# Optimization experiments

Hardware: AMD Instinct MI355X
Metric: run time of the kernel (lower is better)

Reference implementation:

```python
import jax, jax.numpy as jnp
import numpy as np

D_MODEL = 1024
N_HEADS = 16
HEAD_DIM = D_MODEL // N_HEADS  # 64
SCALE = HEAD_DIM ** -0.5       # nn.Parameter, frozen since lsa=False


def setup_inputs() -> dict:
    key = jax.random.key(0)
    kq, kk, kv = jax.random.split(key, 3)
    bs, h, s, d = 4, N_HEADS, 2048, HEAD_DIM
    q = jax.random.normal(kq, (bs, h, s, d), dtype=jnp.float32)
    k = jax.random.normal(kk, (bs, h, d, s), dtype=jnp.float32)  # pre-transposed like torch input
    v = jax.random.normal(kv, (bs, h, s, d), dtype=jnp.float32)
    return {"q": q, "k": k, "v": v}


def reference(q, k, v):
    # attn_scores: [bs, n_heads, q_len, seq_len]
    scale = jnp.asarray(SCALE, dtype=q.dtype)
    attn_scores = jnp.einsum('bhqd,bhds->bhqs', q, k) * scale
    # prev=None, attn_mask=None, key_padding_mask=None; dropout p=0.0 -> identity
    attn_weights = jax.nn.softmax(attn_scores, axis=-1)
    output = jnp.einsum('bhqs,bhsd->bhqd', attn_weights, v)
    return output, attn_weights
```

## Files before the change

### kernel.cpp

```cpp
#include <hip/hip_runtime.h>


#define S_LEN 2048
#define DH 64
#define NHEADS 64

typedef short short8 __attribute__((ext_vector_type(8)));
typedef float f32x4 __attribute__((ext_vector_type(4)));
typedef float f32x16 __attribute__((ext_vector_type(16)));
typedef unsigned short u16;

__device__ __forceinline__ u16 f2bf(float f) {
  union { float f; unsigned u; } x;
  x.f = f;
  unsigned r = x.u + 0x7fffu + ((x.u >> 16) & 1u);
  return (u16)(r >> 16);
}

__device__ __forceinline__ unsigned pkbf(float a, float b) {
  return (unsigned)f2bf(a) | ((unsigned)f2bf(b) << 16);
}

__device__ __forceinline__ void plswap(unsigned& a, unsigned& b) {
  asm("v_permlane32_swap_b32 %0, %1" : "+v"(a), "+v"(b));
}

__global__ __launch_bounds__(256) void cvt_scale_k(const float* __restrict__ in,
                                                   u16* __restrict__ out,
                                                   float scale, int n4) {
  int i = blockIdx.x * 256 + threadIdx.x;
  if (i >= n4) return;
  float4 v = ((const float4*)in)[i];
  union { u16 s[4]; unsigned long long ll; } o;
  o.s[0] = f2bf(v.x * scale); o.s[1] = f2bf(v.y * scale);
  o.s[2] = f2bf(v.z * scale); o.s[3] = f2bf(v.w * scale);
  ((unsigned long long*)out)[i] = o.ll;
}

__global__ __launch_bounds__(256) void transpose_cvt_k(const float* __restrict__ in,
                                                       u16* __restrict__ out,
                                                       int R, int C) {
  __shared__ float tile[64][65];
  const int tilesC = C >> 6;
  const int tilesPerHead = (R >> 6) * tilesC;
  int hb = blockIdx.x;
  int head = hb / tilesPerHead;
  int t = hb - head * tilesPerHead;
  int tr = t / tilesC, tc = t - tr * tilesC;
  const float* ip = in + (size_t)head * R * C + (size_t)tr * 64 * C + (size_t)tc * 64;
  u16* op = out + (size_t)head * R * C + (size_t)tc * 64 * R + (size_t)tr * 64;
  int c = threadIdx.x & 63, r0 = threadIdx.x >> 6;
#pragma unroll
  for (int k = 0; k < 16; ++k) {
    int r = (k << 2) + r0;
    tile[r][c] = ip[(size_t)r * C + c];
  }
  __syncthreads();
#pragma unroll
  for (int k = 0; k < 16; ++k) {
    int orow = (k << 2) + r0;
    op[(size_t)orow * R + c] = f2bf(tile[c][orow]);
  }
}

__global__ __launch_bounds__(256, 2) void attn_k(const u16* __restrict__ Qb,
                                                 const u16* __restrict__ Kn,
                                                 const u16* __restrict__ Vt,
                                                 float* __restrict__ Og,
                                                 float* __restrict__ Pg) {
  __shared__ float tile[4][32 * 32];
  int bid = blockIdx.x;
  int work = ((bid & 7) << 6) | (bid >> 3);
  int head = work >> 3;
  int rblk = work & 7;
  int lane = threadIdx.x & 63;
  int wv = threadIdx.x >> 6;
  int q = lane & 31;
  int hi = lane >> 5;
  int q0A = (rblk << 8) + (wv << 5);
  int q0B = q0A + 128;
  float* tw = tile[wv];
  int rq = lane >> 3;
  int rc = lane & 7;

  const u16* qpA = Qb + (size_t)(head * S_LEN + q0A + q) * DH + hi * 8;
  short8 qa0 = *(const short8*)(qpA);
  short8 qa1 = *(const short8*)(qpA + 16);
  short8 qa2 = *(const short8*)(qpA + 32);
  short8 qa3 = *(const short8*)(qpA + 48);
  const u16* qpB = Qb + (size_t)(head * S_LEN + q0B + q) * DH + hi * 8;
  short8 qb0 = *(const short8*)(qpB);
  short8 qb1 = *(const short8*)(qpB + 16);
  short8 qb2 = *(const short8*)(qpB + 32);
  short8 qb3 = *(const short8*)(qpB + 48);

  const u16* kp = Kn + (size_t)head * S_LEN * DH + (size_t)q * DH + hi * 8;
  const u16* vp = Vt + (size_t)head * DH * S_LEN + (size_t)q * S_LEN + hi * 8;

  float la0 = 0.f, la1 = 0.f, la2 = 0.f, la3 = 0.f;
  for (int j0 = 0; j0 < S_LEN; j0 += 32) {
    const u16* kb = kp + (size_t)j0 * DH;
    short8 k0 = *(const short8*)(kb);
    short8 k1 = *(const short8*)(kb + 16);
    short8 k2 = *(const short8*)(kb + 32);
    short8 k3 = *(const short8*)(kb + 48);
    f32x16 s = {};
    s = __builtin_amdgcn_mfma_f32_32x32x16_bf16(k0, qa0, s, 0, 0, 0);
    s = __builtin_amdgcn_mfma_f32_32x32x16_bf16(k1, qa1, s, 0, 0, 0);
    s = __builtin_amdgcn_mfma_f32_32x32x16_bf16(k2, qa2, s, 0, 0, 0);
    s = __builtin_amdgcn_mfma_f32_32x32x16_bf16(k3, qa3, s, 0, 0, 0);
#pragma unroll
    for (int r = 0; r < 16; r += 4) {
      la0 += __expf(s[r]);
      la1 += __expf(s[r + 1]);
      la2 += __expf(s[r + 2]);
      la3 += __expf(s[r + 3]);
    }
  }
  float lsA = (la0 + la1) + (la2 + la3);
  lsA += __shfl_xor(lsA, 32);
  float rlA = 1.f / lsA;

  f32x16 oa = {}, ob = {};
  float lb0 = 0.f, lb1 = 0.f, lb2 = 0.f, lb3 = 0.f;
  float* pbA = Pg + (size_t)(head * S_LEN + q0A) * S_LEN;

  for (int j0 = 0; j0 < S_LEN; j0 += 32) {
    const u16* kb = kp + (size_t)j0 * DH;
    short8 k0 = *(const short8*)(kb);
    short8 k1 = *(const short8*)(kb + 16);
    short8 k2 = *(const short8*)(kb + 32);
    short8 k3 = *(const short8*)(kb + 48);
    const u16* vj = vp + j0;
    short8 v0 = *(const short8*)(vj);
    short8 v1 = *(const short8*)(vj + 16);
    short8 v2 = *(const short8*)(vj + 32 * S_LEN);
    short8 v3 = *(const short8*)(vj + 32 * S_LEN + 16);

    f32x16 s = {};
    s = __builtin_amdgcn_mfma_f32_32x32x16_bf16(k0, qa0, s, 0, 0, 0);
    s = __builtin_amdgcn_mfma_f32_32x32x16_bf16(k1, qa1, s, 0, 0, 0);
    s = __builtin_amdgcn_mfma_f32_32x32x16_bf16(k2, qa2, s, 0, 0, 0);
    s = __builtin_amdgcn_mfma_f32_32x32x16_bf16(k3, qa3, s, 0, 0, 0);

    float p[16];
#pragma unroll
    for (int r = 0; r < 16; ++r) p[r] = __expf(s[r]) * rlA;

#pragma unroll
    for (int g = 0; g < 4; ++g) {
      int phys = (2 * g + hi) ^ (q & 7);
      f32x4 w = {p[4 * g], p[4 * g + 1], p[4 * g + 2], p[4 * g + 3]};
      *(f32x4*)&tw[q * 32 + phys * 4] = w;
    }

    unsigned A0 = pkbf(p[0], p[1]),   A1 = pkbf(p[2], p[3]);
    unsigned B0 = pkbf(p[4], p[5]),   B1 = pkbf(p[6], p[7]);
    plswap(A0, B0);
    plswap(A1, B1);
    unsigned C0 = pkbf(p[8], p[9]),   C1 = pkbf(p[10], p[11]);
    unsigned D0 = pkbf(p[12], p[13]), D1 = pkbf(p[14], p[15]);
    plswap(C0, D0);
    plswap(C1, D1);
    union { unsigned w[4]; short8 v; } pa0u = {{A0, A1, B0, B1}};
    union { unsigned w[4]; short8 v; } pa1u = {{C0, C1, D0, D1}};

    oa = __builtin_amdgcn_mfma_f32_32x32x16_bf16(pa0u.v, v0, oa, 0, 0, 0);
    oa = __builtin_amdgcn_mfma_f32_32x32x16_bf16(pa1u.v, v1, oa, 0, 0, 0);
    ob = __builtin_amdgcn_mfma_f32_32x32x16_bf16(pa0u.v, v2, ob, 0, 0, 0);
    ob = __builtin_amdgcn_mfma_f32_32x32x16_bf16(pa1u.v, v3, ob, 0, 0, 0);

    float* ps = pbA + j0;
#pragma unroll
    for (int g = 0; g < 4; ++g) {
      int qi = 8 * g + rq;
      int phys = rc ^ (qi & 7);
      f32x4 v = *(const f32x4*)&tw[qi * 32 + phys * 4];
      __builtin_nontemporal_store(v, (f32x4*)(ps + (size_t)qi * S_LEN + rc * 4));
    }

    f32x16 sb = {};
    sb = __builtin_amdgcn_mfma_f32_32x32x16_bf16(k0, qb0, sb, 0, 0, 0);
    sb = __builtin_amdgcn_mfma_f32_32x32x16_bf16(k1, qb1, sb, 0, 0, 0);
    sb = __builtin_amdgcn_mfma_f32_32x32x16_bf16(k2, qb2, sb, 0, 0, 0);
    sb = __builtin_amdgcn_mfma_f32_32x32x16_bf16(k3, qb3, sb, 0, 0, 0);
#pragma unroll
    for (int r = 0; r < 16; r += 4) {
      lb0 += __expf(sb[r]);
      lb1 += __expf(sb[r + 1]);
      lb2 += __expf(sb[r + 2]);
      lb3 += __expf(sb[r + 3]);
    }
  }

  float* ogA = Og + (size_t)(head * S_LEN + q0A) * DH;
#pragma unroll
  for (int r = 0; r < 16; ++r) {
    int qi = (r & 3) + 8 * (r >> 2) + 4 * hi;
    tw[qi * 32 + q] = oa[r];
  }
#pragma unroll
  for (int g = 0; g < 4; ++g) {
    int qi = 8 * g + rq;
    f32x4 v = *(const f32x4*)&tw[qi * 32 + rc * 4];
    __builtin_nontemporal_store(v, (f32x4*)(ogA + (size_t)qi * DH + rc * 4));
  }
#pragma unroll
  for (int r = 0; r < 16; ++r) {
    int qi = (r & 3) + 8 * (r >> 2) + 4 * hi;
    tw[qi * 32 + q] = ob[r];
  }
#pragma unroll
  for (int g = 0; g < 4; ++g) {
    int qi = 8 * g + rq;
    f32x4 v = *(const f32x4*)&tw[qi * 32 + rc * 4];
    __builtin_nontemporal_store(v, (f32x4*)(ogA + (size_t)qi * DH + 32 + rc * 4));
  }

  float lsB = (lb0 + lb1) + (lb2 + lb3);
  lsB += __shfl_xor(lsB, 32);
  float rlB = 1.f / lsB;

  oa = (f32x16){};
  ob = (f32x16){};
  float* pbB = Pg + (size_t)(head * S_LEN + q0B) * S_LEN;

  for (int j0 = 0; j0 < S_LEN; j0 += 32) {
    const u16* kb = kp + (size_t)j0 * DH;
    short8 k0 = *(const short8*)(kb);
    short8 k1 = *(const short8*)(kb + 16);
    short8 k2 = *(const short8*)(kb + 32);
    short8 k3 = *(const short8*)(kb + 48);
    const u16* vj = vp + j0;
    short8 v0 = *(const short8*)(vj);
    short8 v1 = *(const short8*)(vj + 16);
    short8 v2 = *(const short8*)(vj + 32 * S_LEN);
    short8 v3 = *(const short8*)(vj + 32 * S_LEN + 16);

    f32x16 s = {};
    s = __builtin_amdgcn_mfma_f32_32x32x16_bf16(k0, qb0, s, 0, 0, 0);
    s = __builtin_amdgcn_mfma_f32_32x32x16_bf16(k1, qb1, s, 0, 0, 0);
    s = __builtin_amdgcn_mfma_f32_32x32x16_bf16(k2, qb2, s, 0, 0, 0);
    s = __builtin_amdgcn_mfma_f32_32x32x16_bf16(k3, qb3, s, 0, 0, 0);

    float p[16];
#pragma unroll
    for (int r = 0; r < 16; ++r) p[r] = __expf(s[r]) * rlB;

#pragma unroll
    for (int g = 0; g < 4; ++g) {
      int phys = (2 * g + hi) ^ (q & 7);
      f32x4 w = {p[4 * g], p[4 * g + 1], p[4 * g + 2], p[4 * g + 3]};
      *(f32x4*)&tw[q * 32 + phys * 4] = w;
    }

    unsigned A0 = pkbf(p[0], p[1]),   A1 = pkbf(p[2], p[3]);
    unsigned B0 = pkbf(p[4], p[5]),   B1 = pkbf(p[6], p[7]);
    plswap(A0, B0);
    plswap(A1, B1);
    unsigned C0 = pkbf(p[8], p[9]),   C1 = pkbf(p[10], p[11]);
    unsigned D0 = pkbf(p[12], p[13]), D1 = pkbf(p[14], p[15]);
    plswap(C0, D0);
    plswap(C1, D1);
    union { unsigned w[4]; short8 v; } pa0u = {{A0, A1, B0, B1}};
    union { unsigned w[4]; short8 v; } pa1u = {{C0, C1, D0, D1}};

    oa = __builtin_amdgcn_mfma_f32_32x32x16_bf16(pa0u.v, v0, oa, 0, 0, 0);
    oa = __builtin_amdgcn_mfma_f32_32x32x16_bf16(pa1u.v, v1, oa, 0, 0, 0);
    ob = __builtin_amdgcn_mfma_f32_32x32x16_bf16(pa0u.v, v2, ob, 0, 0, 0);
    ob = __builtin_amdgcn_mfma_f32_32x32x16_bf16(pa1u.v, v3, ob, 0, 0, 0);

    float* ps = pbB + j0;
#pragma unroll
    for (int g = 0; g < 4; ++g) {
      int qi = 8 * g + rq;
      int phys = rc ^ (qi & 7);
      f32x4 v = *(const f32x4*)&tw[qi * 32 + phys * 4];
      __builtin_nontemporal_store(v, (f32x4*)(ps + (size_t)qi * S_LEN + rc * 4));
    }
  }

  float* ogB = Og + (size_t)(head * S_LEN + q0B) * DH;
#pragma unroll
  for (int r = 0; r < 16; ++r) {
    int qi = (r & 3) + 8 * (r >> 2) + 4 * hi;
    tw[qi * 32 + q] = oa[r];
  }
#pragma unroll
  for (int g = 0; g < 4; ++g) {
    int qi = 8 * g + rq;
    f32x4 v = *(const f32x4*)&tw[qi * 32 + rc * 4];
    __builtin_nontemporal_store(v, (f32x4*)(ogB + (size_t)qi * DH + rc * 4));
  }
#pragma unroll
  for (int r = 0; r < 16; ++r) {
    int qi = (r & 3) + 8 * (r >> 2) + 4 * hi;
    tw[qi * 32 + q] = ob[r];
  }
#pragma unroll
  for (int g = 0; g < 4; ++g) {
    int qi = 8 * g + rq;
    f32x4 v = *(const f32x4*)&tw[qi * 32 + rc * 4];
    __builtin_nontemporal_store(v, (f32x4*)(ogB + (size_t)qi * DH + 32 + rc * 4));
  }
}

extern "C" void kernel_launch(void* const* d_in, const int* in_sizes, int n_in,
                              void* d_out, int out_size, void* d_ws, size_t ws_size,
                              hipStream_t stream) {
  const float* q = (const float*)d_in[0];
  const float* k = (const float*)d_in[1];
  const float* v = (const float*)d_in[2];
  float* Og = (float*)d_out;
  float* Pg = Og + (size_t)NHEADS * S_LEN * DH;

  const size_t elems = (size_t)NHEADS * S_LEN * DH;
  u16* Qb = (u16*)d_ws;
  u16* Kn = Qb + elems;
  u16* Vt = Kn + elems;

  int n4 = (int)(elems / 4);
  cvt_scale_k<<<n4 / 256, 256, 0, stream>>>(q, Qb, 0.125f, n4);
  transpose_cvt_k<<<NHEADS * (S_LEN / 64), 256, 0, stream>>>(k, Kn, DH, S_LEN);
  transpose_cvt_k<<<NHEADS * (S_LEN / 64), 256, 0, stream>>>(v, Vt, S_LEN, DH);
  attn_k<<<NHEADS * (S_LEN / 256), 256, 0, stream>>>(Qb, Kn, Vt, Og, Pg);
}
```

Before: 350.2 us.

## Merge preprocessing kernels into one launch and hoist second score MFMA

```diff
diff --git a/kernel.cpp b/kernel.cpp
--- a/kernel.cpp
+++ b/kernel.cpp
@@ -25,25 +25,33 @@
   asm("v_permlane32_swap_b32 %0, %1" : "+v"(a), "+v"(b));
 }
 
-__global__ __launch_bounds__(256) void cvt_scale_k(const float* __restrict__ in,
-                                                   u16* __restrict__ out,
-                                                   float scale, int n4) {
-  int i = blockIdx.x * 256 + threadIdx.x;
-  if (i >= n4) return;
-  float4 v = ((const float4*)in)[i];
-  union { u16 s[4]; unsigned long long ll; } o;
-  o.s[0] = f2bf(v.x * scale); o.s[1] = f2bf(v.y * scale);
-  o.s[2] = f2bf(v.z * scale); o.s[3] = f2bf(v.w * scale);
-  ((unsigned long long*)out)[i] = o.ll;
-}
-
-__global__ __launch_bounds__(256) void transpose_cvt_k(const float* __restrict__ in,
-                                                       u16* __restrict__ out,
-                                                       int R, int C) {
+__global__ __launch_bounds__(256) void prep_k(const float* __restrict__ qin,
+                                              const float* __restrict__ kin,
+                                              const float* __restrict__ vin,
+                                              u16* __restrict__ Qb,
+                                              u16* __restrict__ Kn,
+                                              u16* __restrict__ Vt) {
   __shared__ float tile[64][65];
+  int b = blockIdx.x;
+  if (b < 8192) {
+    int i = b * 256 + threadIdx.x;
+    float4 v = ((const float4*)qin)[i];
+    union { u16 s[4]; unsigned long long ll; } o;
+    o.s[0] = f2bf(v.x * 0.125f); o.s[1] = f2bf(v.y * 0.125f);
+    o.s[2] = f2bf(v.z * 0.125f); o.s[3] = f2bf(v.w * 0.125f);
+    ((unsigned long long*)Qb)[i] = o.ll;
+    return;
+  }
+  const float* in;
+  u16* out;
+  int R, C, hb;
+  if (b < 10240) {
+    in = kin; out = Kn; R = DH; C = S_LEN; hb = b - 8192;
+  } else {
+    in = vin; out = Vt; R = S_LEN; C = DH; hb = b - 10240;
+  }
   const int tilesC = C >> 6;
   const int tilesPerHead = (R >> 6) * tilesC;
-  int hb = blockIdx.x;
   int head = hb / tilesPerHead;
   int t = hb - head * tilesPerHead;
   int tr = t / tilesC, tc = t - tr * tilesC;
@@ -170,6 +178,19 @@
     ob = __builtin_amdgcn_mfma_f32_32x32x16_bf16(pa0u.v, v2, ob, 0, 0, 0);
     ob = __builtin_amdgcn_mfma_f32_32x32x16_bf16(pa1u.v, v3, ob, 0, 0, 0);
 
+    f32x16 sb = {};
+    sb = __builtin_amdgcn_mfma_f32_32x32x16_bf16(k0, qb0, sb, 0, 0, 0);
+    sb = __builtin_amdgcn_mfma_f32_32x32x16_bf16(k1, qb1, sb, 0, 0, 0);
+    sb = __builtin_amdgcn_mfma_f32_32x32x16_bf16(k2, qb2, sb, 0, 0, 0);
+    sb = __builtin_amdgcn_mfma_f32_32x32x16_bf16(k3, qb3, sb, 0, 0, 0);
+#pragma unroll
+    for (int r = 0; r < 16; r += 4) {
+      lb0 += __expf(sb[r]);
+      lb1 += __expf(sb[r + 1]);
+      lb2 += __expf(sb[r + 2]);
+      lb3 += __expf(sb[r + 3]);
+    }
+
     float* ps = pbA + j0;
 #pragma unroll
     for (int g = 0; g < 4; ++g) {
@@ -177,19 +198,6 @@
       int phys = rc ^ (qi & 7);
       f32x4 v = *(const f32x4*)&tw[qi * 32 + phys * 4];
       __builtin_nontemporal_store(v, (f32x4*)(ps + (size_t)qi * S_LEN + rc * 4));
-    }
-
-    f32x16 sb = {};
-    sb = __builtin_amdgcn_mfma_f32_32x32x16_bf16(k0, qb0, sb, 0, 0, 0);
-    sb = __builtin_amdgcn_mfma_f32_32x32x16_bf16(k1, qb1, sb, 0, 0, 0);
-    sb = __builtin_amdgcn_mfma_f32_32x32x16_bf16(k2, qb2, sb, 0, 0, 0);
-    sb = __builtin_amdgcn_mfma_f32_32x32x16_bf16(k3, qb3, sb, 0, 0, 0);
-#pragma unroll
-    for (int r = 0; r < 16; r += 4) {
-      lb0 += __expf(sb[r]);
-      lb1 += __expf(sb[r + 1]);
-      lb2 += __expf(sb[r + 2]);
-      lb3 += __expf(sb[r + 3]);
     }
   }
 
@@ -319,9 +327,6 @@
   u16* Kn = Qb + elems;
   u16* Vt = Kn + elems;
 
-  int n4 = (int)(elems / 4);
-  cvt_scale_k<<<n4 / 256, 256, 0, stream>>>(q, Qb, 0.125f, n4);
-  transpose_cvt_k<<<NHEADS * (S_LEN / 64), 256, 0, stream>>>(k, Kn, DH, S_LEN);
-  transpose_cvt_k<<<NHEADS * (S_LEN / 64), 256, 0, stream>>>(v, Vt, S_LEN, DH);
+  prep_k<<<12288, 256, 0, stream>>>(q, k, v, Qb, Kn, Vt);
   attn_k<<<NHEADS * (S_LEN / 256), 256, 0, stream>>>(Qb, Kn, Vt, Og, Pg);
 }
```

New measurement: 346.5 us. About the same (-1.1%).
